# Kernel tuning notes

Measured on AMD Instinct MI355X. Metric: run time of the kernel, lower is better.

## Reference

```python
import jax, jax.numpy as jnp
import numpy as np

ID, IH, IW = 8, 16, 16
HEADS, DIM_HEAD = 8, 32
INP, OUP = 256, 256
B = 4
N = ID * IH * IW  # 2048
INNER = HEADS * DIM_HEAD  # 256
SCALE = DIM_HEAD ** -0.5


def _make_relative_pos():
    # Faithful to the torch ctor: 3D coords, pairwise diffs, linearize, shift to >=0
    z, y, x = np.meshgrid(np.arange(ID), np.arange(IH), np.arange(IW), indexing='ij')
    coords = np.stack([z.ravel(), y.ravel(), x.ravel()], axis=1)  # [N,3]
    rel = coords[:, None, :] - coords[None, :, :]                 # [N,N,3]
    rp = rel[:, :, 0] * (IH * IW) + rel[:, :, 1] * IW + rel[:, :, 2]
    rp = rp - rp.min()
    return jnp.asarray(rp, dtype=jnp.int32)                       # [N,N]


def setup_inputs() -> dict:
    key = jax.random.key(0)
    k1, k2, k3, k4, k5 = jax.random.split(key, 5)
    table_size = ID * IH * IW * 8  # 16384, as in nn.Embedding ctor
    return {
        "x": jax.random.normal(k1, (B, N, INP), dtype=jnp.float32),
        "w_qkv": jax.random.normal(k2, (INP, 3 * INNER), dtype=jnp.float32) * (INP ** -0.5),
        "bias_table": jax.random.normal(k3, (table_size, 1), dtype=jnp.float32),
        "w_out": jax.random.normal(k4, (INNER, OUP), dtype=jnp.float32) * (INNER ** -0.5),
        "b_out": jax.random.normal(k5, (OUP,), dtype=jnp.float32),
        "relative_pos": _make_relative_pos(),
    }


def reference(x, w_qkv, bias_table, w_out, b_out, relative_pos):
    Bb, Nn, C = x.shape
    qkv = x @ w_qkv                                   # [B, N, 3*H*D]
    qkv = qkv.reshape(Bb, Nn, 3, HEADS, DIM_HEAD)
    qkv = jnp.transpose(qkv, (2, 0, 3, 1, 4))         # [3, B, H, N, D]
    q, k, v = qkv[0], qkv[1], qkv[2]
    q = q * SCALE
    attn = jnp.einsum('bhnd,bhmd->bhnm', q, k)        # [B, H, N, N]
    bias = bias_table[relative_pos, 0]                # [N, N], shared across B,H
    attn = attn + bias
    attn = jax.nn.softmax(attn, axis=-1)
    out = jnp.einsum('bhnm,bhmd->bhnd', attn, v)      # [B, H, N, D]
    out = jnp.transpose(out, (0, 2, 1, 3)).reshape(Bb, Nn, INNER)
    return out @ w_out + b_out                        # dropout p=0 -> identity
```

## Files before the change

kernel.cpp:

```cpp
#include <hip/hip_runtime.h>

typedef unsigned short u16;
typedef unsigned int u32;
typedef __attribute__((ext_vector_type(8))) short bf16x8;
typedef __attribute__((ext_vector_type(4))) short bf16x4;
typedef __attribute__((ext_vector_type(4))) float f32x4;

#define MFMA16(a, b, c) __builtin_amdgcn_mfma_f32_16x16x32_bf16(a, b, c, 0, 0, 0)
#define MFMAK16(a, b, c) __builtin_amdgcn_mfma_f32_16x16x16bf16_1k(a, b, c, 0, 0, 0)

__device__ __forceinline__ float hw_exp2(float x) { return __builtin_amdgcn_exp2f(x); }

__device__ __forceinline__ u16 f2bf(float f) {
    union { float f; u32 i; } v; v.f = f;
    u32 x = v.i;
    return (u16)((x + 0x7FFFu + ((x >> 16) & 1u)) >> 16);
}

__global__ __launch_bounds__(256) void k_prep(const float* __restrict__ x,
                                              const float* __restrict__ wqkv,
                                              const float* __restrict__ wout,
                                              u16* __restrict__ xb,
                                              u16* __restrict__ wqkvT,
                                              u16* __restrict__ woutT) {
    const float QSCALE2 = 0.2550566756538019f;
    int bx = blockIdx.x, tid = threadIdx.x;
    if (bx < 1024) {
        int base = bx * 2048 + tid * 8;
        float4 a = *(const float4*)(x + base);
        float4 b = *(const float4*)(x + base + 4);
        uint4 r;
        r.x = f2bf(a.x) | ((u32)f2bf(a.y) << 16);
        r.y = f2bf(a.z) | ((u32)f2bf(a.w) << 16);
        r.z = f2bf(b.x) | ((u32)f2bf(b.y) << 16);
        r.w = f2bf(b.z) | ((u32)f2bf(b.w) << 16);
        *(uint4*)(xb + base) = r;
    } else if (bx < 1792) {
        int idx = (bx - 1024) * 256 + tid;
        int n = idx >> 8, kk = idx & 255;
        float sc = (n < 256) ? QSCALE2 : 1.0f;
        wqkvT[idx] = f2bf(wqkv[kk * 768 + n] * sc);
    } else {
        int idx = (bx - 1792) * 256 + tid;
        int n = idx >> 8, kk = idx & 255;
        woutT[idx] = f2bf(wout[kk * 256 + n]);
    }
}

__global__ __launch_bounds__(256) void k_gemm_qkv(const u16* __restrict__ xb,
                                                  const u16* __restrict__ wT,
                                                  u16* __restrict__ qkv) {
    __shared__ __align__(16) u16 slds[8704];
    const int tid = threadIdx.x;
    const int wave = tid >> 6, lane = tid & 63, quad = lane >> 4, ql = lane & 15;
    const int mbase = blockIdx.x * 128 + (wave & 1) * 64;
    const int nbase = blockIdx.y * 64 + (wave >> 1) * 32;
    f32x4 acc[4][2];
#pragma unroll
    for (int i = 0; i < 4; ++i)
#pragma unroll
        for (int j = 0; j < 2; ++j) acc[i][j] = (f32x4){0.f, 0.f, 0.f, 0.f};
#pragma unroll
    for (int ks = 0; ks < 8; ++ks) {
        bf16x8 af[4], bfm[2];
#pragma unroll
        for (int ms = 0; ms < 4; ++ms)
            af[ms] = *(const bf16x8*)(xb + (size_t)(mbase + ms * 16 + ql) * 256 + ks * 32 + quad * 8);
#pragma unroll
        for (int ns = 0; ns < 2; ++ns)
            bfm[ns] = *(const bf16x8*)(wT + (size_t)(nbase + ns * 16 + ql) * 256 + ks * 32 + quad * 8);
#pragma unroll
        for (int ms = 0; ms < 4; ++ms)
#pragma unroll
            for (int ns = 0; ns < 2; ++ns)
                acc[ms][ns] = MFMA16(af[ms], bfm[ns], acc[ms][ns]);
    }

    const int t = (blockIdx.y * 64) >> 8;
    if (t < 2) {
        const int rowb = (wave & 1) * 64, colb = (wave >> 1) * 32;
#pragma unroll
        for (int ms = 0; ms < 4; ++ms)
#pragma unroll
            for (int ns = 0; ns < 2; ++ns)
#pragma unroll
                for (int r = 0; r < 4; ++r)
                    slds[(rowb + ms * 16 + quad * 4 + r) * 68 + colb + ns * 16 + ql] =
                        f2bf(acc[ms][ns][r]);
        __syncthreads();
        u16* base = qkv + (size_t)t * 2097152;
#pragma unroll
        for (int p = 0; p < 8; ++p) {
            int c = p * 256 + tid;
            int row = c >> 4, ch = c & 15;
            uint2 w = *(const uint2*)&slds[row * 68 + ch * 4];
            int n = blockIdx.x * 128 + row;
            int col = blockIdx.y * 64 + ch * 4;
            int h = (col & 255) >> 5, d = col & 31;
            *(uint2*)(base + ((size_t)((n >> 11) * 8 + h) * 2048 + (n & 2047)) * 32 + d) = w;
        }
    } else {
        const int hl = wave >> 1, nb = (wave & 1) * 64;
#pragma unroll
        for (int ms = 0; ms < 4; ++ms)
#pragma unroll
            for (int ns = 0; ns < 2; ++ns) {
                u16 e0 = f2bf(acc[ms][ns][0]), e1 = f2bf(acc[ms][ns][1]);
                u16 e2 = f2bf(acc[ms][ns][2]), e3 = f2bf(acc[ms][ns][3]);
                uint2 pp; pp.x = e0 | ((u32)e1 << 16); pp.y = e2 | ((u32)e3 << 16);
                *(uint2*)&slds[(hl * 32 + ns * 16 + ql) * 136 + nb + ms * 16 + quad * 4] = pp;
            }
        __syncthreads();
        u16* vbase = qkv + (size_t)2 * 2097152;
#pragma unroll
        for (int p = 0; p < 4; ++p) {
            int c = p * 256 + tid;
            int row = c >> 4, ch = c & 15;
            bf16x8 w = *(const bf16x8*)&slds[row * 136 + ch * 8];
            int n0 = blockIdx.x * 128 + ch * 8;
            int h = (blockIdx.y & 3) * 2 + (row >> 5), d = row & 31;
            *(bf16x8*)(vbase + (size_t)((n0 >> 11) * 8 + h) * 65536 +
                       (size_t)d * 2048 + (n0 & 2047)) = w;
        }
    }
}

__global__ __launch_bounds__(256, 2) void k_attn(const u16* __restrict__ q,
                                                 const u16* __restrict__ k,
                                                 const u16* __restrict__ vT,
                                                 const float* __restrict__ table,
                                                 u16* __restrict__ att) {
    __shared__ __align__(16) u16 kbuf[2][2][2048];
    __shared__ __align__(16) u16 vbuf[2][2][2048];
    __shared__ float tbl2[2176];
    const int tid = threadIdx.x;
    const int bh = blockIdx.x & 31, qt = blockIdx.x >> 5;
    const int wave = tid >> 6, lane = tid & 63, quad = lane >> 4, ql = lane & 15;
    const float LOG2E = 1.4426950408889634f;

    const u16* kbh = k + (size_t)bh * 65536;
    const u16* vbh = vT + (size_t)bh * 65536;

    const int krow = wave * 16 + (lane >> 2);
    const u16* kg = kbh + krow * 32 + ((((lane & 3) ^ ((lane >> 3) & 3))) << 3);
    const int vd = wave * 8 + (lane >> 3);
    const u16* vg = vbh + (size_t)vd * 2048 + (((lane & 7) ^ (vd & 7)) << 3);

#define GLDS(SRC, DST) __builtin_amdgcn_global_load_lds(                         \
        (const __attribute__((address_space(1))) void*)(SRC),                    \
        (__attribute__((address_space(3))) void*)(DST), 16, 0, 0)
#define DMA(BUF, PAIR) do {                                                      \
    GLDS(kg + (PAIR) * 4096,        &kbuf[BUF][0][wave * 512]);                  \
    GLDS(kg + (PAIR) * 4096 + 2048, &kbuf[BUF][1][wave * 512]);                  \
    GLDS(vg + (PAIR) * 128,         &vbuf[BUF][0][wave * 512]);                  \
    GLDS(vg + (PAIR) * 128 + 64,    &vbuf[BUF][1][wave * 512]);                  \
} while (0)

    DMA(0, 0);

    const float4* tg = (const float4*)(table + qt * 128);
    for (int i = tid; i < 544; i += 256) {
        float4 t = tg[i];
        t.x *= LOG2E; t.y *= LOG2E; t.z *= LOG2E; t.w *= LOG2E;
        ((float4*)tbl2)[i] = t;
    }

    const int qr0 = qt * 128 + wave * 32 + ql;
    bf16x8 qf[2];
    qf[0] = *(const bf16x8*)(q + ((size_t)bh * 2048 + qr0) * 32 + quad * 8);
    qf[1] = *(const bf16x8*)(q + ((size_t)bh * 2048 + qr0 + 16) * 32 + quad * 8);
    const int bloc0 = wave * 32 + ql + 2047 - quad * 4;
    const int kro = ((quad ^ ((ql >> 1) & 3)) << 3);

    bf16x4 ones4;
#pragma unroll
    for (int i = 0; i < 4; ++i) ones4[i] = (short)0x3F80;

    f32x4 oT0[2], oT1[2], oL[2];
#pragma unroll
    for (int qh = 0; qh < 2; ++qh) {
        oT0[qh] = (f32x4){0.f, 0.f, 0.f, 0.f};
        oT1[qh] = (f32x4){0.f, 0.f, 0.f, 0.f};
        oL[qh]  = (f32x4){0.f, 0.f, 0.f, 0.f};
    }

    __syncthreads();

    for (int pr = 0; pr < 16; ++pr) {
        const int buf = pr & 1;
        if (pr < 15) DMA(buf ^ 1, pr + 1);

#pragma unroll
        for (int t = 0; t < 2; ++t) {
            const int kt = pr * 2 + t;
            const u16* kb = &kbuf[buf][t][0];
            const u16* vb = &vbuf[buf][t][0];
            bf16x8 kf[4];
            bf16x4 va[2][4];
#pragma unroll
            for (int j = 0; j < 4; ++j)
                kf[j] = *(const bf16x8*)(kb + (j * 16 + ql) * 32 + kro);
#pragma unroll
            for (int dt = 0; dt < 2; ++dt)
#pragma unroll
                for (int j = 0; j < 4; ++j) {
                    int nloc = j * 16 + quad * 4;
                    int slot = (nloc >> 3) ^ (ql & 7);
                    va[dt][j] = *(const bf16x4*)(vb + (dt * 16 + ql) * 64 +
                                                 slot * 8 + (nloc & 7));
                }
            const int bkt = bloc0 - kt * 64;
            float bg[5][4];
#pragma unroll
            for (int g = 0; g < 5; ++g)
#pragma unroll
                for (int r = 0; r < 4; ++r)
                    bg[g][r] = tbl2[bkt + 16 * g - 48 - r];

#pragma unroll
            for (int qh = 0; qh < 2; ++qh) {
                f32x4 z = {0.f, 0.f, 0.f, 0.f};
                f32x4 s[4];
#pragma unroll
                for (int j = 0; j < 4; ++j) s[j] = MFMA16(kf[j], qf[qh], z);
#pragma unroll
                for (int j = 0; j < 4; ++j)
#pragma unroll
                    for (int r = 0; r < 4; ++r)
                        s[j][r] = hw_exp2(s[j][r] + bg[qh + 3 - j][r]);
#pragma unroll
                for (int j = 0; j < 4; ++j) {
                    union { u32 u[2]; bf16x4 v; } pj;
                    pj.u[0] = __builtin_amdgcn_perm(__float_as_uint(s[j][1]),
                                                    __float_as_uint(s[j][0]), 0x07060302u);
                    pj.u[1] = __builtin_amdgcn_perm(__float_as_uint(s[j][3]),
                                                    __float_as_uint(s[j][2]), 0x07060302u);
                    oT0[qh] = MFMAK16(va[0][j], pj.v, oT0[qh]);
                    oT1[qh] = MFMAK16(va[1][j], pj.v, oT1[qh]);
                    oL[qh]  = MFMAK16(ones4, pj.v, oL[qh]);
                }
            }
        }
        __syncthreads();
    }
#undef DMA
#undef GLDS

#pragma unroll
    for (int qh = 0; qh < 2; ++qh) {
        float inv = 1.0f / oL[qh][0];
        size_t base = ((size_t)bh * 2048 + qr0 + qh * 16) * 32;
#pragma unroll
        for (int dt = 0; dt < 2; ++dt) {
            const f32x4& o = dt ? oT1[qh] : oT0[qh];
            u16 e0 = f2bf(o[0] * inv), e1 = f2bf(o[1] * inv);
            u16 e2 = f2bf(o[2] * inv), e3 = f2bf(o[3] * inv);
            uint2 pp; pp.x = e0 | ((u32)e1 << 16); pp.y = e2 | ((u32)e3 << 16);
            *(uint2*)(att + base + dt * 16 + quad * 4) = pp;
        }
    }
}

__global__ __launch_bounds__(256) void k_gemm_out(const u16* __restrict__ attq,
                                                  const u16* __restrict__ wT,
                                                  const float* __restrict__ bout,
                                                  float* __restrict__ out) {
    const int tid = threadIdx.x;
    const int wave = tid >> 6, lane = tid & 63, quad = lane >> 4, ql = lane & 15;
    const int mbase = blockIdx.x * 128 + (wave & 1) * 64;
    const int nbase = blockIdx.y * 64 + (wave >> 1) * 32;
    f32x4 acc[4][2];
#pragma unroll
    for (int i = 0; i < 4; ++i)
#pragma unroll
        for (int j = 0; j < 2; ++j) acc[i][j] = (f32x4){0.f, 0.f, 0.f, 0.f};
#pragma unroll
    for (int ks = 0; ks < 8; ++ks) {
        bf16x8 af[4], bfm[2];
#pragma unroll
        for (int ms = 0; ms < 4; ++ms) {
            int row = mbase + ms * 16 + ql;
            af[ms] = *(const bf16x8*)(attq +
                ((size_t)((row >> 11) * 8 + ks) * 2048 + (row & 2047)) * 32 + quad * 8);
        }
#pragma unroll
        for (int ns = 0; ns < 2; ++ns)
            bfm[ns] = *(const bf16x8*)(wT + (size_t)(nbase + ns * 16 + ql) * 256 + ks * 32 + quad * 8);
#pragma unroll
        for (int ms = 0; ms < 4; ++ms)
#pragma unroll
            for (int ns = 0; ns < 2; ++ns)
                acc[ms][ns] = MFMA16(af[ms], bfm[ns], acc[ms][ns]);
    }
#pragma unroll
    for (int ms = 0; ms < 4; ++ms)
#pragma unroll
        for (int ns = 0; ns < 2; ++ns)
#pragma unroll
            for (int r = 0; r < 4; ++r) {
                int Mrow = mbase + ms * 16 + quad * 4 + r;
                int col = nbase + ns * 16 + ql;
                out[(size_t)Mrow * 256 + col] = acc[ms][ns][r] + bout[col];
            }
}

extern "C" void kernel_launch(void* const* d_in, const int* in_sizes, int n_in,
                              void* d_out, int out_size, void* d_ws, size_t ws_size,
                              hipStream_t stream) {
    const float* x    = (const float*)d_in[0];
    const float* wqkv = (const float*)d_in[1];
    const float* btab = (const float*)d_in[2];
    const float* wout = (const float*)d_in[3];
    const float* bout = (const float*)d_in[4];
    float* out = (float*)d_out;

    if (ws_size < (size_t)13107200) return;
    u16* ws = (u16*)d_ws;
    u16* wqkvT = ws;
    u16* woutT = wqkvT + 196608;
    u16* qkv   = woutT + 65536;
    u16* xb    = (u16*)d_out;

    hipLaunchKernelGGL(k_prep, dim3(2048), dim3(256), 0, stream, x, wqkv, wout, xb, wqkvT, woutT);
    hipLaunchKernelGGL(k_gemm_qkv, dim3(64, 12), dim3(256), 0, stream, xb, wqkvT, qkv);
    hipLaunchKernelGGL(k_attn, dim3(512), dim3(256), 0, stream,
                       qkv, qkv + 2097152, qkv + 2 * 2097152, btab, qkv);
    hipLaunchKernelGGL(k_gemm_out, dim3(64, 4), dim3(256), 0, stream, qkv, woutT, bout, out);
}
```

Before: 141.6 us.

## Split attention key range across two blocks and combine partials in a new kernel

Each attention block now handles half of the key sequence, which doubles the grid to 1024 blocks. Each block writes unnormalised fp32 output partials and row sums to workspace. A new combine kernel adds the two halves, normalises, and writes the bf16 attention output. The bias-table slice in shared memory shrinks and launch bounds allow 4 blocks per CU, both aimed at better GPU occupancy. The cost is an extra kernel launch and extra global traffic for the fp32 partials.

```diff
diff --git a/kernel.cpp b/kernel.cpp
--- a/kernel.cpp
+++ b/kernel.cpp
@@ -125,16 +125,17 @@
     }
 }
 
-__global__ __launch_bounds__(256, 2) void k_attn(const u16* __restrict__ q,
+__global__ __launch_bounds__(256, 4) void k_attn(const u16* __restrict__ q,
                                                  const u16* __restrict__ k,
                                                  const u16* __restrict__ vT,
                                                  const float* __restrict__ table,
-                                                 u16* __restrict__ att) {
+                                                 float* __restrict__ Opart,
+                                                 float* __restrict__ lpart) {
     __shared__ __align__(16) u16 kbuf[2][2][2048];
     __shared__ __align__(16) u16 vbuf[2][2][2048];
-    __shared__ float tbl2[2176];
+    __shared__ float tbl2[1160];
     const int tid = threadIdx.x;
-    const int bh = blockIdx.x & 31, qt = blockIdx.x >> 5;
+    const int bh = blockIdx.x & 31, qt = (blockIdx.x >> 5) & 15, kh = blockIdx.x >> 9;
     const int wave = tid >> 6, lane = tid & 63, quad = lane >> 4, ql = lane & 15;
     const float LOG2E = 1.4426950408889634f;
 
@@ -142,9 +143,9 @@
     const u16* vbh = vT + (size_t)bh * 65536;
 
     const int krow = wave * 16 + (lane >> 2);
-    const u16* kg = kbh + krow * 32 + ((((lane & 3) ^ ((lane >> 3) & 3))) << 3);
+    const u16* kg = kbh + kh * 32768 + krow * 32 + ((((lane & 3) ^ ((lane >> 3) & 3))) << 3);
     const int vd = wave * 8 + (lane >> 3);
-    const u16* vg = vbh + (size_t)vd * 2048 + (((lane & 7) ^ (vd & 7)) << 3);
+    const u16* vg = vbh + (size_t)vd * 2048 + kh * 1024 + (((lane & 7) ^ (vd & 7)) << 3);
 
 #define GLDS(SRC, DST) __builtin_amdgcn_global_load_lds(                         \
         (const __attribute__((address_space(1))) void*)(SRC),                    \
@@ -158,8 +159,8 @@
 
     DMA(0, 0);
 
-    const float4* tg = (const float4*)(table + qt * 128);
-    for (int i = tid; i < 544; i += 256) {
+    const float4* tg = (const float4*)(table + qt * 128 - kh * 1024 + 1024);
+    for (int i = tid; i < 288; i += 256) {
         float4 t = tg[i];
         t.x *= LOG2E; t.y *= LOG2E; t.z *= LOG2E; t.w *= LOG2E;
         ((float4*)tbl2)[i] = t;
@@ -169,7 +170,7 @@
     bf16x8 qf[2];
     qf[0] = *(const bf16x8*)(q + ((size_t)bh * 2048 + qr0) * 32 + quad * 8);
     qf[1] = *(const bf16x8*)(q + ((size_t)bh * 2048 + qr0 + 16) * 32 + quad * 8);
-    const int bloc0 = wave * 32 + ql + 2047 - quad * 4;
+    const int bloc0 = wave * 32 + ql + 1023 - quad * 4;
     const int kro = ((quad ^ ((ql >> 1) & 3)) << 3);
 
     bf16x4 ones4;
@@ -186,13 +187,13 @@
 
     __syncthreads();
 
-    for (int pr = 0; pr < 16; ++pr) {
+    for (int pr = 0; pr < 8; ++pr) {
         const int buf = pr & 1;
-        if (pr < 15) DMA(buf ^ 1, pr + 1);
+        if (pr < 7) DMA(buf ^ 1, pr + 1);
 
 #pragma unroll
         for (int t = 0; t < 2; ++t) {
-            const int kt = pr * 2 + t;
+            const int ktl = pr * 2 + t;
             const u16* kb = &kbuf[buf][t][0];
             const u16* vb = &vbuf[buf][t][0];
             bf16x8 kf[4];
@@ -209,7 +210,7 @@
                     va[dt][j] = *(const bf16x4*)(vb + (dt * 16 + ql) * 64 +
                                                  slot * 8 + (nloc & 7));
                 }
-            const int bkt = bloc0 - kt * 64;
+            const int bkt = bloc0 - ktl * 64;
             float bg[5][4];
 #pragma unroll
             for (int g = 0; g < 5; ++g)
@@ -246,19 +247,39 @@
 #undef DMA
 #undef GLDS
 
+    float* Ob = Opart + (size_t)kh * 2097152 + (size_t)bh * 65536;
 #pragma unroll
     for (int qh = 0; qh < 2; ++qh) {
-        float inv = 1.0f / oL[qh][0];
-        size_t base = ((size_t)bh * 2048 + qr0 + qh * 16) * 32;
+        int row = qr0 + qh * 16;
 #pragma unroll
         for (int dt = 0; dt < 2; ++dt) {
             const f32x4& o = dt ? oT1[qh] : oT0[qh];
-            u16 e0 = f2bf(o[0] * inv), e1 = f2bf(o[1] * inv);
-            u16 e2 = f2bf(o[2] * inv), e3 = f2bf(o[3] * inv);
-            uint2 pp; pp.x = e0 | ((u32)e1 << 16); pp.y = e2 | ((u32)e3 << 16);
-            *(uint2*)(att + base + dt * 16 + quad * 4) = pp;
-        }
-    }
+            float4 w; w.x = o[0]; w.y = o[1]; w.z = o[2]; w.w = o[3];
+            *(float4*)(Ob + (size_t)row * 32 + dt * 16 + quad * 4) = w;
+        }
+        if (quad == 0)
+            lpart[(size_t)kh * 65536 + (size_t)bh * 2048 + row] = oL[qh][0];
+    }
+}
+
+__global__ __launch_bounds__(256) void k_comb(const float* __restrict__ Opart,
+                                              const float* __restrict__ lpart,
+                                              u16* __restrict__ att) {
+    int idx = blockIdx.x * 256 + threadIdx.x;
+    int bh = idx >> 13, rem = idx & 8191;
+    int qrow = rem >> 2, dq = (rem & 3) * 8;
+    size_t o0 = (size_t)bh * 65536 + qrow * 32 + dq;
+    float4 a0 = *(const float4*)(Opart + o0);
+    float4 a1 = *(const float4*)(Opart + o0 + 4);
+    float4 b0 = *(const float4*)(Opart + 2097152 + o0);
+    float4 b1 = *(const float4*)(Opart + 2097152 + o0 + 4);
+    float inv = 1.0f / (lpart[bh * 2048 + qrow] + lpart[65536 + bh * 2048 + qrow]);
+    uint4 r;
+    r.x = f2bf((a0.x + b0.x) * inv) | ((u32)f2bf((a0.y + b0.y) * inv) << 16);
+    r.y = f2bf((a0.z + b0.z) * inv) | ((u32)f2bf((a0.w + b0.w) * inv) << 16);
+    r.z = f2bf((a1.x + b1.x) * inv) | ((u32)f2bf((a1.y + b1.y) * inv) << 16);
+    r.w = f2bf((a1.z + b1.z) * inv) | ((u32)f2bf((a1.w + b1.w) * inv) << 16);
+    *(uint4*)(att + o0) = r;
 }
 
 __global__ __launch_bounds__(256) void k_gemm_out(const u16* __restrict__ attq,
@@ -314,16 +335,19 @@
     const float* bout = (const float*)d_in[4];
     float* out = (float*)d_out;
 
-    if (ws_size < (size_t)13107200) return;
+    if (ws_size < (size_t)30408704) return;
     u16* ws = (u16*)d_ws;
     u16* wqkvT = ws;
     u16* woutT = wqkvT + 196608;
     u16* qkv   = woutT + 65536;
+    float* Opart = (float*)(qkv + 3 * 2097152);
+    float* lpart = Opart + 4194304;
     u16* xb    = (u16*)d_out;
 
     hipLaunchKernelGGL(k_prep, dim3(2048), dim3(256), 0, stream, x, wqkv, wout, xb, wqkvT, woutT);
     hipLaunchKernelGGL(k_gemm_qkv, dim3(64, 12), dim3(256), 0, stream, xb, wqkvT, qkv);
-    hipLaunchKernelGGL(k_attn, dim3(512), dim3(256), 0, stream,
-                       qkv, qkv + 2097152, qkv + 2 * 2097152, btab, qkv);
+    hipLaunchKernelGGL(k_attn, dim3(1024), dim3(256), 0, stream,
+                       qkv, qkv + 2097152, qkv + 2 * 2097152, btab, Opart, lpart);
+    hipLaunchKernelGGL(k_comb, dim3(1024), dim3(256), 0, stream, Opart, lpart, qkv);
     hipLaunchKernelGGL(k_gemm_out, dim3(64, 4), dim3(256), 0, stream, qkv, woutT, bout, out);
 }
```

Measured after the change: 142.3 us. No clear change (+0.5%).
